# Kernel optimization log

Measured on AMD Instinct MI355X. Metric: run time of the kernel, lower is better.

Reference implementation:

```python
import jax, jax.numpy as jnp
import numpy as np

N_NODES = 100000


def setup_inputs() -> dict:
    key = jax.random.key(0)
    k1, k2, k3, k4 = jax.random.split(key, 4)
    N, E, D_IN, D_OUT = N_NODES, 3200000, 256, 256
    feature = jax.random.normal(k1, (N, D_IN), dtype=jnp.float32)
    edge_src = jax.random.randint(k2, (E,), 0, N, dtype=jnp.int32)
    edge_dst = jax.random.randint(k3, (E,), 0, N, dtype=jnp.int32)
    W = jax.random.normal(k4, (D_IN, D_OUT), dtype=jnp.float32) * (1.0 / np.sqrt(D_IN))
    b = jnp.zeros((D_OUT,), dtype=jnp.float32)
    return {"feature": feature, "edge_src": edge_src, "edge_dst": edge_dst, "W": W, "b": b}


def reference(feature, edge_src, edge_dst, W, b):
    # update_all(copy_src('h','m'), sum('m','h')): for each node i,
    # h_i = sum over edges (j->i) of feature[j]  -- scatter-add by destination.
    msgs = feature[edge_src]                                   # [E, D_in] (gather)
    agg = jax.ops.segment_sum(msgs, edge_dst, num_segments=N_NODES)  # [N, D_in]
    # apply_nodes: Linear + activation (relu)
    h = jnp.dot(agg, W) + b                                    # [N, D_out]
    return jax.nn.relu(h)
```

## Files before the change

### kernel.cpp

```cpp
#include <hip/hip_runtime.h>

#define D 256
#define GSHIFT 4
#define GSIZE 16
#define KMAX4 6400
#define NB_P 256
#define TN 16
#define CAPG 2048

using bf16x8 = __attribute__((ext_vector_type(8))) short;
using f32x4  = __attribute__((ext_vector_type(4))) float;

__device__ inline float bf_lo(unsigned int u) {
    return __builtin_bit_cast(float, u << 16);
}
__device__ inline float bf_hi(unsigned int u) {
    return __builtin_bit_cast(float, u & 0xffff0000u);
}
__device__ inline unsigned short f2bf(float f) {
    unsigned int x = __builtin_bit_cast(unsigned int, f);
    unsigned int r = (x + 0x7fffu + ((x >> 16) & 1u)) >> 16;
    return (unsigned short)r;
}

__global__ __launch_bounds__(256) void part_kernel(
    const int* __restrict__ src, const int* __restrict__ dst,
    int* __restrict__ gcnt, int* __restrict__ csrPacked,
    const float* __restrict__ feature, unsigned short* __restrict__ fbf, long n8,
    const float* __restrict__ W, unsigned short* __restrict__ Wt,
    int E, int K, int chunk, int nConvF)
{
    __shared__ int h[KMAX4];
    const int b = blockIdx.x, t = threadIdx.x;

    if (b < NB_P) {
        for (int i = t; i < K; i += 256) h[i] = 0;
        __syncthreads();
        const int beg = b * chunk;
        const int end = min(beg + chunk, E);
        for (int i = beg + t; i < end; i += 256)
            atomicAdd(&h[dst[i] >> GSHIFT], 1);
        __syncthreads();
        for (int i = t; i < K; i += 256) {
            int c = h[i];
            h[i] = c ? atomicAdd(&gcnt[i], c) : 0;
        }
        __syncthreads();
        for (int i = beg + t; i < end; i += 256) {
            int d = dst[i];
            int k = d >> GSHIFT;
            int r = atomicAdd(&h[k], 1);
            if (r < CAPG)
                csrPacked[(size_t)k * CAPG + r] = (src[i] << GSHIFT) | (d & (GSIZE - 1));
        }
        return;
    }
    if (b < NB_P + nConvF) {
        long i = (long)(b - NB_P) * 256 + t;
        if (i < n8) {
            const float4* p = reinterpret_cast<const float4*>(feature + i * 8);
            float4 v0 = p[0], v1 = p[1];
            uint4 r;
            r.x = (unsigned int)f2bf(v0.x) | ((unsigned int)f2bf(v0.y) << 16);
            r.y = (unsigned int)f2bf(v0.z) | ((unsigned int)f2bf(v0.w) << 16);
            r.z = (unsigned int)f2bf(v1.x) | ((unsigned int)f2bf(v1.y) << 16);
            r.w = (unsigned int)f2bf(v1.z) | ((unsigned int)f2bf(v1.w) << 16);
            *reinterpret_cast<uint4*>(fbf + i * 8) = r;
        }
        return;
    }
    int i = (b - NB_P - nConvF) * 256 + t;
    if (i < D * D / 4) {
        int n  = i >> 6;
        int k0 = (i & 63) * 4;
        float a  = W[(size_t)(k0 + 0) * D + n];
        float bb = W[(size_t)(k0 + 1) * D + n];
        float c  = W[(size_t)(k0 + 2) * D + n];
        float d  = W[(size_t)(k0 + 3) * D + n];
        uint2 r;
        r.x = (unsigned int)f2bf(a) | ((unsigned int)f2bf(bb) << 16);
        r.y = (unsigned int)f2bf(c) | ((unsigned int)f2bf(d) << 16);
        *reinterpret_cast<uint2*>(Wt + (size_t)n * D + k0) = r;
    }
}

__global__ __launch_bounds__(256) void agg_gemm_kernel(
    const unsigned short* __restrict__ fbf,
    const int* __restrict__ csrPacked,
    const int* __restrict__ gcnt,
    const unsigned short* __restrict__ Wt,
    const float* __restrict__ bias,
    float* __restrict__ out, int N)
{
    __shared__ int lsrc[CAPG];
    __shared__ int nBeg[TN], nCnt[TN], nCur[TN];
    __shared__ unsigned short A[TN][D + 8];

    const int blk  = blockIdx.x;
    const int t    = threadIdx.x;
    const int wave = t >> 6;
    const int lane = t & 63;
    const int sub  = lane & 31;
    const int half = lane >> 5;
    const int node0 = blk * TN;
    const size_t colOff = (size_t)(sub << 3);

    const size_t beg = (size_t)blk * CAPG;
    const int cnt = min(gcnt[blk], CAPG);

    if (t < TN) nCnt[t] = 0;
    __syncthreads();
    for (int i = t; i < cnt; i += 256)
        atomicAdd(&nCnt[csrPacked[beg + i] & (GSIZE - 1)], 1);
    __syncthreads();
    if (t == 0) {
        int run = 0;
        for (int j = 0; j < TN; ++j) { nBeg[j] = run; run += nCnt[j]; }
    }
    __syncthreads();
    if (t < TN) nCur[t] = nBeg[t];
    __syncthreads();
    for (int i = t; i < cnt; i += 256) {
        int p = csrPacked[beg + i];
        int r = atomicAdd(&nCur[p & (GSIZE - 1)], 1);
        lsrc[r] = p >> GSHIFT;
    }
    __syncthreads();

    for (int ni = 0; ni < 4; ++ni) {
        const int l = (wave << 2) + ni;
        const int node = node0 + l;
        float a0 = 0.f, a1 = 0.f, a2 = 0.f, a3 = 0.f;
        float a4 = 0.f, a5 = 0.f, a6 = 0.f, a7 = 0.f;
        if (node < N) {
            const int b0 = nBeg[l];
            const int c0 = nCnt[l];
            int j = 0;
            for (; j + 3 < c0; j += 4) {
                int s0 = lsrc[b0 + j + half];
                int s1 = lsrc[b0 + j + 2 + half];
                uint4 v0 = *reinterpret_cast<const uint4*>(fbf + ((size_t)s0 << 8) + colOff);
                uint4 v1 = *reinterpret_cast<const uint4*>(fbf + ((size_t)s1 << 8) + colOff);
                a0 += bf_lo(v0.x); a1 += bf_hi(v0.x); a2 += bf_lo(v0.y); a3 += bf_hi(v0.y);
                a4 += bf_lo(v0.z); a5 += bf_hi(v0.z); a6 += bf_lo(v0.w); a7 += bf_hi(v0.w);
                a0 += bf_lo(v1.x); a1 += bf_hi(v1.x); a2 += bf_lo(v1.y); a3 += bf_hi(v1.y);
                a4 += bf_lo(v1.z); a5 += bf_hi(v1.z); a6 += bf_lo(v1.w); a7 += bf_hi(v1.w);
            }
            if (j + 1 < c0) {
                int s0 = lsrc[b0 + j + half];
                uint4 v0 = *reinterpret_cast<const uint4*>(fbf + ((size_t)s0 << 8) + colOff);
                a0 += bf_lo(v0.x); a1 += bf_hi(v0.x); a2 += bf_lo(v0.y); a3 += bf_hi(v0.y);
                a4 += bf_lo(v0.z); a5 += bf_hi(v0.z); a6 += bf_lo(v0.w); a7 += bf_hi(v0.w);
                j += 2;
            }
            if (j < c0 && half == 0) {
                int s0 = lsrc[b0 + j];
                uint4 v0 = *reinterpret_cast<const uint4*>(fbf + ((size_t)s0 << 8) + colOff);
                a0 += bf_lo(v0.x); a1 += bf_hi(v0.x); a2 += bf_lo(v0.y); a3 += bf_hi(v0.y);
                a4 += bf_lo(v0.z); a5 += bf_hi(v0.z); a6 += bf_lo(v0.w); a7 += bf_hi(v0.w);
            }
        }
        a0 += __shfl_xor(a0, 32); a1 += __shfl_xor(a1, 32);
        a2 += __shfl_xor(a2, 32); a3 += __shfl_xor(a3, 32);
        a4 += __shfl_xor(a4, 32); a5 += __shfl_xor(a5, 32);
        a6 += __shfl_xor(a6, 32); a7 += __shfl_xor(a7, 32);
        if (half == 0) {
            uint4 r;
            r.x = (unsigned int)f2bf(a0) | ((unsigned int)f2bf(a1) << 16);
            r.y = (unsigned int)f2bf(a2) | ((unsigned int)f2bf(a3) << 16);
            r.z = (unsigned int)f2bf(a4) | ((unsigned int)f2bf(a5) << 16);
            r.w = (unsigned int)f2bf(a6) | ((unsigned int)f2bf(a7) << 16);
            *reinterpret_cast<uint4*>(&A[l][sub << 3]) = r;
        }
    }
    __syncthreads();

    const int lr = lane & 15;
    const int lg = lane >> 4;

    bf16x8 afr[8];
#pragma unroll
    for (int ks = 0; ks < 8; ++ks)
        afr[ks] = *reinterpret_cast<const bf16x8*>(&A[lr][ks * 32 + lg * 8]);

#pragma unroll
    for (int c = 0; c < 4; ++c) {
        const int ct = (wave << 2) + c;
        f32x4 acc = {0.f, 0.f, 0.f, 0.f};
        const unsigned short* bp = Wt + (size_t)(ct * 16 + lr) * D + lg * 8;
#pragma unroll
        for (int ks = 0; ks < 8; ++ks) {
            bf16x8 bfr = *reinterpret_cast<const bf16x8*>(bp + ks * 32);
            acc = __builtin_amdgcn_mfma_f32_16x16x32_bf16(afr[ks], bfr, acc, 0, 0, 0);
        }
        const float bv = bias[ct * 16 + lr];
#pragma unroll
        for (int jj = 0; jj < 4; ++jj) {
            int row = node0 + lg * 4 + jj;
            if (row < N) {
                float v = acc[jj] + bv;
                out[(size_t)row * D + ct * 16 + lr] = v > 0.f ? v : 0.f;
            }
        }
    }
}

__global__ __launch_bounds__(256) void scatter_kernel(
    const float* __restrict__ feature, const int* __restrict__ src,
    const int* __restrict__ dst, float* __restrict__ agg, int E)
{
    int edge = blockIdx.x * (blockDim.x >> 6) + (threadIdx.x >> 6);
    int lane = threadIdx.x & 63;
    if (edge >= E) return;
    int s = src[edge];
    int d = dst[edge];
    const float4 v = *reinterpret_cast<const float4*>(feature + (size_t)s * D + lane * 4);
    float* o = agg + (size_t)d * D + lane * 4;
    atomicAdd(o + 0, v.x);
    atomicAdd(o + 1, v.y);
    atomicAdd(o + 2, v.z);
    atomicAdd(o + 3, v.w);
}

#define BM 32
__global__ __launch_bounds__(256) void linear_relu_kernel(
    float* __restrict__ h, const float* __restrict__ W,
    const float* __restrict__ b, int n_nodes)
{
    __shared__ float sA[BM][D];
    const int node0 = blockIdx.x * BM;
    const int t = threadIdx.x;
    for (int m = 0; m < BM; ++m) {
        int nd = node0 + m;
        sA[m][t] = (nd < n_nodes) ? h[(size_t)nd * D + t] : 0.0f;
    }
    __syncthreads();
    float acc[BM];
#pragma unroll
    for (int m = 0; m < BM; ++m) acc[m] = 0.0f;
    for (int kk = 0; kk < D; ++kk) {
        float w = W[kk * D + t];
#pragma unroll
        for (int m = 0; m < BM; ++m) acc[m] += sA[m][kk] * w;
    }
    const float bias = b[t];
    for (int m = 0; m < BM; ++m) {
        int nd = node0 + m;
        if (nd < n_nodes) {
            float v = acc[m] + bias;
            h[(size_t)nd * D + t] = v > 0.0f ? v : 0.0f;
        }
    }
}

extern "C" void kernel_launch(void* const* d_in, const int* in_sizes, int n_in,
                              void* d_out, int out_size, void* d_ws, size_t ws_size,
                              hipStream_t stream)
{
    const float* feature = (const float*)d_in[0];
    const int*   src     = (const int*)d_in[1];
    const int*   dst     = (const int*)d_in[2];
    const float* W       = (const float*)d_in[3];
    const float* b       = (const float*)d_in[4];
    float*       out     = (float*)d_out;

    const int E = in_sizes[1];
    const int N = in_sizes[0] / D;
    const int K = (N + GSIZE - 1) >> GSHIFT;
    const int chunk = (E + NB_P - 1) / NB_P;

    size_t off = 0;
    auto alloc = [&](size_t bytes, size_t align) {
        off = (off + align - 1) / align * align;
        size_t r = off; off += bytes; return r;
    };
    size_t o_gcnt   = alloc((size_t)K * 4, 16);
    size_t o_packed = alloc((size_t)K * CAPG * 4, 16);
    size_t o_wt     = alloc((size_t)D * D * 2, 16);
    size_t o_fbf    = alloc((size_t)N * D * 2, 16);
    size_t need_full = off;

    char* ws = (char*)d_ws;

    const bool cap_ok = ((long)E / K) * 2 + 64 <= CAPG;

    if (ws_size >= need_full && K <= KMAX4 && cap_ok) {
        int* gcnt      = (int*)(ws + o_gcnt);
        int* csrPacked = (int*)(ws + o_packed);
        unsigned short* Wt  = (unsigned short*)(ws + o_wt);
        unsigned short* fbf = (unsigned short*)(ws + o_fbf);

        const long n8 = (long)N * D / 8;
        const int nConvF = (int)((n8 + 255) / 256);
        const int nConvW = (D * D / 4 + 255) / 256;

        hipMemsetAsync(gcnt, 0, (size_t)K * 4, stream);

        part_kernel<<<NB_P + nConvF + nConvW, 256, 0, stream>>>(
            src, dst, gcnt, csrPacked, feature, fbf, n8, W, Wt,
            E, K, chunk, nConvF);

        agg_gemm_kernel<<<(N + TN - 1) / TN, 256, 0, stream>>>(
            fbf, csrPacked, gcnt, Wt, b, out, N);
    } else {
        hipMemsetAsync(d_out, 0, (size_t)out_size * sizeof(float), stream);
        scatter_kernel<<<(E + 3) / 4, 256, 0, stream>>>(feature, src, dst, out, E);
        linear_relu_kernel<<<(N + BM - 1) / BM, 256, 0, stream>>>(out, W, b, N);
    }
}
```

Measured before the change: 408.7 us.

## Split edge partitioning into coarse 256-node bins plus a per-bin regroup pass

The single-pass partition into 6250 fine groups of 16 nodes is replaced by a two-level bucketing. Edges are first binned into 391 coarse bins of 256 nodes using a small shared histogram, and a new regroup kernel then sorts each bin into its 16 fine groups. The aim is to cut the large shared-memory histogram and the global atomics and scattered writes in the partition pass, giving better occupancy and more coalesced writes. The cost is an extra kernel launch and an additional read and write pass over the edge list through a second workspace buffer.

```diff
diff --git a/kernel.cpp b/kernel.cpp
--- a/kernel.cpp
+++ b/kernel.cpp
@@ -3,10 +3,14 @@
 #define D 256
 #define GSHIFT 4
 #define GSIZE 16
-#define KMAX4 6400
+#define TN 16
+#define CAPG2 1024
+#define CSHIFT 8
+#define CBIN 256
+#define GPB 16
+#define NCMAX 512
+#define CAPC 9216
 #define NB_P 256
-#define TN 16
-#define CAPG 2048
 
 using bf16x8 = __attribute__((ext_vector_type(8))) short;
 using f32x4  = __attribute__((ext_vector_type(4))) float;
@@ -25,33 +29,33 @@
 
 __global__ __launch_bounds__(256) void part_kernel(
     const int* __restrict__ src, const int* __restrict__ dst,
-    int* __restrict__ gcnt, int* __restrict__ csrPacked,
+    int* __restrict__ gcntC, int* __restrict__ csrA,
     const float* __restrict__ feature, unsigned short* __restrict__ fbf, long n8,
     const float* __restrict__ W, unsigned short* __restrict__ Wt,
-    int E, int K, int chunk, int nConvF)
-{
-    __shared__ int h[KMAX4];
+    int E, int NC, int chunk, int nConvF)
+{
+    __shared__ int h[NCMAX];
     const int b = blockIdx.x, t = threadIdx.x;
 
     if (b < NB_P) {
-        for (int i = t; i < K; i += 256) h[i] = 0;
+        for (int i = t; i < NC; i += 256) h[i] = 0;
         __syncthreads();
         const int beg = b * chunk;
         const int end = min(beg + chunk, E);
         for (int i = beg + t; i < end; i += 256)
-            atomicAdd(&h[dst[i] >> GSHIFT], 1);
+            atomicAdd(&h[dst[i] >> CSHIFT], 1);
         __syncthreads();
-        for (int i = t; i < K; i += 256) {
+        for (int i = t; i < NC; i += 256) {
             int c = h[i];
-            h[i] = c ? atomicAdd(&gcnt[i], c) : 0;
+            h[i] = c ? atomicAdd(&gcntC[i], c) : 0;
         }
         __syncthreads();
         for (int i = beg + t; i < end; i += 256) {
             int d = dst[i];
-            int k = d >> GSHIFT;
-            int r = atomicAdd(&h[k], 1);
-            if (r < CAPG)
-                csrPacked[(size_t)k * CAPG + r] = (src[i] << GSHIFT) | (d & (GSIZE - 1));
+            int c = d >> CSHIFT;
+            int r = atomicAdd(&h[c], 1);
+            if (r < CAPC)
+                csrA[(size_t)c * CAPC + r] = (src[i] << CSHIFT) | (d & (CBIN - 1));
         }
         return;
     }
@@ -84,15 +88,57 @@
     }
 }
 
+__global__ __launch_bounds__(256) void regroup_kernel(
+    const int* __restrict__ csrA, const int* __restrict__ gcntC,
+    int* __restrict__ csrB, int* __restrict__ gcnt, int K)
+{
+    __shared__ int sorted[CAPC];
+    __shared__ int h2[GPB], b2[GPB], cur2[GPB];
+    const int c = blockIdx.x, t = threadIdx.x;
+    const size_t rbeg = (size_t)c * CAPC;
+    const int cnt = min(gcntC[c], CAPC);
+
+    if (t < GPB) h2[t] = 0;
+    __syncthreads();
+    for (int i = t; i < cnt; i += 256)
+        atomicAdd(&h2[(csrA[rbeg + i] >> GSHIFT) & (GPB - 1)], 1);
+    __syncthreads();
+    if (t == 0) {
+        int run = 0;
+        for (int j = 0; j < GPB; ++j) { b2[j] = run; run += h2[j]; }
+    }
+    __syncthreads();
+    if (t < GPB) cur2[t] = b2[t];
+    __syncthreads();
+    for (int i = t; i < cnt; i += 256) {
+        int p = csrA[rbeg + i];
+        int r = atomicAdd(&cur2[(p >> GSHIFT) & (GPB - 1)], 1);
+        sorted[r] = p;
+    }
+    __syncthreads();
+    for (int i = t; i < cnt; i += 256) {
+        int p = sorted[i];
+        int g = (p >> GSHIFT) & (GPB - 1);
+        int k = (c << 4) + g;
+        int off = i - b2[g];
+        if (k < K && off < CAPG2)
+            csrB[(size_t)k * CAPG2 + off] = ((p >> CSHIFT) << GSHIFT) | (p & (GSIZE - 1));
+    }
+    if (t < GPB) {
+        int k = (c << 4) + t;
+        if (k < K) gcnt[k] = min(h2[t], CAPG2);
+    }
+}
+
 __global__ __launch_bounds__(256) void agg_gemm_kernel(
     const unsigned short* __restrict__ fbf,
-    const int* __restrict__ csrPacked,
+    const int* __restrict__ csrB,
     const int* __restrict__ gcnt,
     const unsigned short* __restrict__ Wt,
     const float* __restrict__ bias,
     float* __restrict__ out, int N)
 {
-    __shared__ int lsrc[CAPG];
+    __shared__ int lsrc[CAPG2];
     __shared__ int nBeg[TN], nCnt[TN], nCur[TN];
     __shared__ unsigned short A[TN][D + 8];
 
@@ -105,13 +151,13 @@
     const int node0 = blk * TN;
     const size_t colOff = (size_t)(sub << 3);
 
-    const size_t beg = (size_t)blk * CAPG;
-    const int cnt = min(gcnt[blk], CAPG);
+    const size_t beg = (size_t)blk * CAPG2;
+    const int cnt = min(gcnt[blk], CAPG2);
 
     if (t < TN) nCnt[t] = 0;
     __syncthreads();
     for (int i = t; i < cnt; i += 256)
-        atomicAdd(&nCnt[csrPacked[beg + i] & (GSIZE - 1)], 1);
+        atomicAdd(&nCnt[csrB[beg + i] & (GSIZE - 1)], 1);
     __syncthreads();
     if (t == 0) {
         int run = 0;
@@ -121,7 +167,7 @@
     if (t < TN) nCur[t] = nBeg[t];
     __syncthreads();
     for (int i = t; i < cnt; i += 256) {
-        int p = csrPacked[beg + i];
+        int p = csrB[beg + i];
         int r = atomicAdd(&nCur[p & (GSIZE - 1)], 1);
         lsrc[r] = p >> GSHIFT;
     }
@@ -266,7 +312,8 @@
 
     const int E = in_sizes[1];
     const int N = in_sizes[0] / D;
-    const int K = (N + GSIZE - 1) >> GSHIFT;
+    const int K  = (N + GSIZE - 1) >> GSHIFT;
+    const int NC = (N + CBIN - 1) >> CSHIFT;
     const int chunk = (E + NB_P - 1) / NB_P;
 
     size_t off = 0;
@@ -274,19 +321,28 @@
         off = (off + align - 1) / align * align;
         size_t r = off; off += bytes; return r;
     };
-    size_t o_gcnt   = alloc((size_t)K * 4, 16);
-    size_t o_packed = alloc((size_t)K * CAPG * 4, 16);
-    size_t o_wt     = alloc((size_t)D * D * 2, 16);
-    size_t o_fbf    = alloc((size_t)N * D * 2, 16);
+    size_t o_gcntC = alloc((size_t)NC * 4, 16);
+    size_t o_csrA  = alloc((size_t)NC * CAPC * 4, 16);
+    size_t o_gcnt  = alloc((size_t)K * 4, 16);
+    size_t o_csrB  = alloc((size_t)K * CAPG2 * 4, 16);
+    size_t o_wt    = alloc((size_t)D * D * 2, 16);
+    size_t o_fbf   = alloc((size_t)N * D * 2, 16);
     size_t need_full = off;
 
     char* ws = (char*)d_ws;
 
-    const bool cap_ok = ((long)E / K) * 2 + 64 <= CAPG;
-
-    if (ws_size >= need_full && K <= KMAX4 && cap_ok) {
-        int* gcnt      = (int*)(ws + o_gcnt);
-        int* csrPacked = (int*)(ws + o_packed);
+    const double mg = (double)E / K;
+    const double mc = (double)E / NC;
+    const bool cap_ok =
+        (mg + 8.0 * __builtin_sqrt(mg) + 16.0 <= (double)CAPG2) &&
+        (mc + 8.0 * __builtin_sqrt(mc) + 16.0 <= (double)CAPC) &&
+        (NC <= NCMAX);
+
+    if (ws_size >= need_full && cap_ok) {
+        int* gcntC = (int*)(ws + o_gcntC);
+        int* csrA  = (int*)(ws + o_csrA);
+        int* gcnt  = (int*)(ws + o_gcnt);
+        int* csrB  = (int*)(ws + o_csrB);
         unsigned short* Wt  = (unsigned short*)(ws + o_wt);
         unsigned short* fbf = (unsigned short*)(ws + o_fbf);
 
@@ -294,14 +350,16 @@
         const int nConvF = (int)((n8 + 255) / 256);
         const int nConvW = (D * D / 4 + 255) / 256;
 
-        hipMemsetAsync(gcnt, 0, (size_t)K * 4, stream);
+        hipMemsetAsync(gcntC, 0, (size_t)NC * 4, stream);
 
         part_kernel<<<NB_P + nConvF + nConvW, 256, 0, stream>>>(
-            src, dst, gcnt, csrPacked, feature, fbf, n8, W, Wt,
-            E, K, chunk, nConvF);
+            src, dst, gcntC, csrA, feature, fbf, n8, W, Wt,
+            E, NC, chunk, nConvF);
+
+        regroup_kernel<<<NC, 256, 0, stream>>>(csrA, gcntC, csrB, gcnt, K);
 
         agg_gemm_kernel<<<(N + TN - 1) / TN, 256, 0, stream>>>(
-            fbf, csrPacked, gcnt, Wt, b, out, N);
+            fbf, csrB, gcnt, Wt, b, out, N);
     } else {
         hipMemsetAsync(d_out, 0, (size_t)out_size * sizeof(float), stream);
         scatter_kernel<<<(E + 3) / 4, 256, 0, stream>>>(feature, src, dst, out, E);
```

Result: faster. 392.0 us (-4.1%).
